# Performance work log

Measured on AMD Instinct MI355X. Metric: run time of the kernel, lower is better.

## Reference

```python
import jax, jax.numpy as jnp
import numpy as np

ALPHA = 1.0
BETA = 1.0


def setup_inputs() -> dict:
    key = jax.random.key(0)
    k1, k2, k3, k4 = jax.random.split(key, 4)
    B_, S, D_in, D_out, R = 4, 64, 8192, 8192, 16
    x = jax.random.normal(k1, (B_, S, D_in), dtype=jnp.float32)
    original_weight = jax.random.normal(k2, (D_out, D_in), dtype=jnp.float32) * 0.02
    A = jax.random.normal(k3, (D_out, R), dtype=jnp.float32) * 0.02
    Bm = jax.random.normal(k4, (R, D_in), dtype=jnp.float32) * 0.02
    return {"x": x, "original_weight": original_weight, "A": A, "B": Bm}


def reference(x, original_weight, A, B):
    # delta_weight = alpha * (A @ B)  -> [D_out, D_in]
    delta_weight = ALPHA * jnp.matmul(A, B)
    # F.linear(x, W + beta*delta) = x @ (W + beta*delta)^T
    W = original_weight + BETA * delta_weight
    return jnp.einsum("bsd,od->bso", x, W)
```

## Files before the change

### kernel.cpp

```cpp
#include <hip/hip_runtime.h>
#include <stdint.h>


#define DM 256
#define DK 8192
#define DN 8192
#define RLORA 16

#define TN 128
#define BK 64
#define KSPLIT 8
#define KCHUNK (DK / KSPLIT)
#define NITER (KCHUNK / BK)

typedef short bf16x8 __attribute__((ext_vector_type(8)));
typedef float f32x4v __attribute__((ext_vector_type(4)));

typedef __attribute__((address_space(1))) const unsigned char glbc_u8;
typedef __attribute__((address_space(3))) unsigned char lds_u8;

__device__ __forceinline__ unsigned short f2bf(float f) {
  unsigned u = __builtin_bit_cast(unsigned, f);
  u += 0x7FFFu + ((u >> 16) & 1u);
  return (unsigned short)(u >> 16);
}

__device__ __forceinline__ bf16x8 pack8(float4 a, float4 b) {
  bf16x8 r;
  r[0] = (short)f2bf(a.x); r[1] = (short)f2bf(a.y);
  r[2] = (short)f2bf(a.z); r[3] = (short)f2bf(a.w);
  r[4] = (short)f2bf(b.x); r[5] = (short)f2bf(b.y);
  r[6] = (short)f2bf(b.z); r[7] = (short)f2bf(b.w);
  return r;
}

__global__ __launch_bounds__(256) void prep_x(
    const float* __restrict__ x, const float* __restrict__ Bm,
    unsigned short* __restrict__ xb, float* __restrict__ y32) {
  const int ks = blockIdx.x;
  const int m0 = blockIdx.y * 4;
  const int t = threadIdx.x;
  const int k0 = ks * 1024 + t * 4;
  float4 xv[4];
#pragma unroll
  for (int i = 0; i < 4; ++i) {
    xv[i] = *(const float4*)(x + (size_t)(m0 + i) * DK + k0);
    ushort4 h;
    h.x = f2bf(xv[i].x); h.y = f2bf(xv[i].y);
    h.z = f2bf(xv[i].z); h.w = f2bf(xv[i].w);
    *(ushort4*)(xb + (size_t)(m0 + i) * DK + k0) = h;
  }
  float acc[4][RLORA];
#pragma unroll
  for (int r = 0; r < RLORA; ++r) {
    float4 b = *(const float4*)(Bm + (size_t)r * DK + k0);
#pragma unroll
    for (int i = 0; i < 4; ++i)
      acc[i][r] = xv[i].x * b.x + xv[i].y * b.y + xv[i].z * b.z + xv[i].w * b.w;
  }
#pragma unroll
  for (int off = 32; off >= 1; off >>= 1)
#pragma unroll
    for (int i = 0; i < 4; ++i)
#pragma unroll
      for (int r = 0; r < RLORA; ++r)
        acc[i][r] += __shfl_xor(acc[i][r], off, 64);
  __shared__ float red[4][4][RLORA];
  const int lane = t & 63, wv = t >> 6;
  if (lane == 0) {
#pragma unroll
    for (int i = 0; i < 4; ++i)
#pragma unroll
      for (int r = 0; r < RLORA; ++r) red[wv][i][r] = acc[i][r];
  }
  __syncthreads();
  if (t < 64) {
    int i = t >> 4, r = t & 15;
    float s = red[0][i][r] + red[1][i][r] + red[2][i][r] + red[3][i][r];
    atomicAdd(y32 + (m0 + i) * RLORA + r, s);
  }
}

__global__ __launch_bounds__(256) void pack_y(
    const float* __restrict__ y32, unsigned short* __restrict__ yb) {
  int e = blockIdx.x * 256 + threadIdx.x;
  int m = e >> 6, c = e & 63;
  yb[e] = (c < RLORA) ? f2bf(y32[m * RLORA + c]) : (unsigned short)0;
}

__global__ __launch_bounds__(512, 4) void lora_gemm(
    const unsigned short* __restrict__ xb,
    const float* __restrict__ W,
    const unsigned short* __restrict__ yb,
    const float* __restrict__ A,
    float* __restrict__ out,
    float* __restrict__ part) {
  __shared__ unsigned short xs[2][DM * BK];

  const int tid = threadIdx.x;
  const int lane = tid & 63;
  const int wave = tid >> 6;
  const int nb = blockIdx.x * TN;
  const int kz = blockIdx.y;
  const int kb = kz * KCHUNK;
  const int n0 = nb + wave * 16;
  const int qr = lane & 15;
  const int quad = lane >> 4;

  const unsigned short* xgp[4];
  unsigned xdst[4];
#pragma unroll
  for (int j = 0; j < 4; ++j) {
    int idx = (wave * 4 + j) * 64 + lane;
    int r = idx & 15, c = (idx >> 4) & 3, s = (idx >> 6) & 1, g = idx >> 7;
    xgp[j] = xb + (size_t)(g * 16 + r) * DK + kb + s * 32 + c * 8;
    xdst[j] = (unsigned)((wave * 4 + j) * 1024);
  }
  const float* wp = W + (size_t)(n0 + qr) * DK + kb + quad * 8;

  f32x4v acc[16];
#pragma unroll
  for (int g = 0; g < 16; ++g) acc[g] = (f32x4v){0.f, 0.f, 0.f, 0.f};

  const bool isLora = (kz == 0);
  const int niter = isLora ? NITER + 1 : NITER;

  float4 f0 = *(const float4*)(wp);
  float4 f1 = *(const float4*)(wp + 4);
  float4 f2 = *(const float4*)(wp + 32);
  float4 f3 = *(const float4*)(wp + 36);
  wp += BK;
#pragma unroll
  for (int j = 0; j < 4; ++j) {
    __builtin_amdgcn_global_load_lds((glbc_u8*)xgp[j],
        (lds_u8*)((char*)&xs[0][0] + xdst[j]), 16, 0, 0);
    xgp[j] += BK;
  }
  __syncthreads();

  for (int it = 0; it < niter; ++it) {
    const int cur = it & 1, nxt = (it + 1) & 1;
    const int ni = it + 1;
    if (ni < NITER) {
#pragma unroll
      for (int j = 0; j < 4; ++j) {
        __builtin_amdgcn_global_load_lds((glbc_u8*)xgp[j],
            (lds_u8*)((char*)&xs[nxt][0] + xdst[j]), 16, 0, 0);
        xgp[j] += BK;
      }
    } else if (ni == NITER && isLora) {
#pragma unroll
      for (int j = 0; j < 4; ++j) {
        int idx = (wave * 4 + j) * 64 + lane;
        int r = idx & 15, c = (idx >> 4) & 3, s = (idx >> 6) & 1, g = idx >> 7;
        const unsigned short* gp = yb + (g * 16 + r) * 64 + s * 32 + c * 8;
        __builtin_amdgcn_global_load_lds((glbc_u8*)gp,
            (lds_u8*)((char*)&xs[nxt][0] + xdst[j]), 16, 0, 0);
      }
    }
    bf16x8 b0 = pack8(f0, f1);
    bf16x8 b1 = pack8(f2, f3);
    if (ni < NITER) {
      f0 = *(const float4*)(wp);
      f1 = *(const float4*)(wp + 4);
      f2 = *(const float4*)(wp + 32);
      f3 = *(const float4*)(wp + 36);
      wp += BK;
    } else if (ni == NITER && isLora) {
      const float* ap = A + (size_t)(n0 + qr) * RLORA + quad * 8;
      float4 z = {0.f, 0.f, 0.f, 0.f};
      f0 = (quad < 2) ? *(const float4*)(ap) : z;
      f1 = (quad < 2) ? *(const float4*)(ap + 4) : z;
      f2 = z; f3 = z;
    }
    const char* xbase = (const char*)&xs[cur][0];
#pragma unroll
    for (int g = 0; g < 16; ++g) {
      bf16x8 a = *(const bf16x8*)(xbase + ((g * 2 + 0) * 64 + lane) * 16);
      acc[g] = __builtin_amdgcn_mfma_f32_16x16x32_bf16(a, b0, acc[g], 0, 0, 0);
    }
#pragma unroll
    for (int g = 0; g < 16; ++g) {
      bf16x8 a = *(const bf16x8*)(xbase + ((g * 2 + 1) * 64 + lane) * 16);
      acc[g] = __builtin_amdgcn_mfma_f32_16x16x32_bf16(a, b1, acc[g], 0, 0, 0);
    }
    __syncthreads();
  }

  if (part) {
    float* pb = part + (size_t)kz * DM * DN + n0 + (lane & 15);
#pragma unroll
    for (int g = 0; g < 16; ++g)
#pragma unroll
      for (int rg = 0; rg < 4; ++rg)
        pb[(size_t)(g * 16 + quad * 4 + rg) * DN] = acc[g][rg];
  } else {
    float* ob = out + n0 + (lane & 15);
#pragma unroll
    for (int g = 0; g < 16; ++g)
#pragma unroll
      for (int rg = 0; rg < 4; ++rg)
        atomicAdd(ob + (size_t)(g * 16 + quad * 4 + rg) * DN, acc[g][rg]);
  }
}

__global__ __launch_bounds__(256) void reduce_k(
    const float* __restrict__ part, float* __restrict__ out) {
  size_t i = ((size_t)blockIdx.x * 256 + threadIdx.x) * 4;
  float4 s = *(const float4*)(part + i);
#pragma unroll
  for (int kz = 1; kz < KSPLIT; ++kz) {
    float4 v = *(const float4*)(part + (size_t)kz * DM * DN + i);
    s.x += v.x; s.y += v.y; s.z += v.z; s.w += v.w;
  }
  *(float4*)(out + i) = s;
}

extern "C" void kernel_launch(void* const* d_in, const int* in_sizes, int n_in,
                              void* d_out, int out_size, void* d_ws, size_t ws_size,
                              hipStream_t stream) {
  const float* x  = (const float*)d_in[0];
  const float* W  = (const float*)d_in[1];
  const float* A  = (const float*)d_in[2];
  const float* Bm = (const float*)d_in[3];
  float* out = (float*)d_out;

  unsigned short* xb = (unsigned short*)d_ws;
  unsigned short* yb = xb + (size_t)DM * DK;
  float* y32 = (float*)(yb + (size_t)DM * 64);
  size_t base_bytes = (size_t)DM * DK * 2 + (size_t)DM * 64 * 2 +
                      (size_t)DM * RLORA * 4;
  size_t part_bytes = (size_t)KSPLIT * DM * DN * 4;
  bool use_part = ws_size >= base_bytes + part_bytes;
  float* part = use_part ? (float*)((char*)d_ws + base_bytes) : nullptr;

  hipMemsetAsync(d_out, 0, (size_t)out_size * sizeof(float), stream);
  hipMemsetAsync(y32, 0, (size_t)DM * RLORA * sizeof(float), stream);
  prep_x<<<dim3(8, 64), 256, 0, stream>>>(x, Bm, xb, y32);
  pack_y<<<64, 256, 0, stream>>>(y32, yb);
  lora_gemm<<<dim3(DN / TN, KSPLIT), 512, 0, stream>>>(xb, W, yb, A, out, part);
  if (use_part) reduce_k<<<2048, 256, 0, stream>>>(part, out);
}
```

Measured before the change: 467.0 us.

## Pre-swizzle x into MFMA fragment layout and drop LDS staging in LoRA GEMM

prep_x now writes bf16 x directly in MFMA A-fragment order, and pack_y does the same for y, so each wave can load its operands straight from global memory without LDS staging or barriers. Each wave now computes a 128x32 output tile over a K chunk, with K split into 4 parts instead of 8. That halves the partial-sum traffic in the reduce, and the output memset is skipped when partials are used. The cost is that the x fragments are re-read from global/L2 by every wave with no LDS sharing across waves, and there are more VGPRs per wave.

```diff
diff --git a/kernel.cpp b/kernel.cpp
--- a/kernel.cpp
+++ b/kernel.cpp
@@ -6,18 +6,13 @@
 #define DK 8192
 #define DN 8192
 #define RLORA 16
-
-#define TN 128
+#define KSPLIT 4
+#define KCHUNK (DK / KSPLIT)
 #define BK 64
-#define KSPLIT 8
-#define KCHUNK (DK / KSPLIT)
 #define NITER (KCHUNK / BK)
 
 typedef short bf16x8 __attribute__((ext_vector_type(8)));
 typedef float f32x4v __attribute__((ext_vector_type(4)));
-
-typedef __attribute__((address_space(1))) const unsigned char glbc_u8;
-typedef __attribute__((address_space(3))) unsigned char lds_u8;
 
 __device__ __forceinline__ unsigned short f2bf(float f) {
   unsigned u = __builtin_bit_cast(unsigned, f);
@@ -40,20 +35,25 @@
   const int ks = blockIdx.x;
   const int m0 = blockIdx.y * 4;
   const int t = threadIdx.x;
-  const int k0 = ks * 1024 + t * 4;
+  const int k = ks * 1024 + t * 4;
+  const int I = k >> 6, s = (k >> 5) & 1, oct = (k >> 3) & 3;
+  const int ebyte = (k & 4) * 2;
   float4 xv[4];
 #pragma unroll
   for (int i = 0; i < 4; ++i) {
-    xv[i] = *(const float4*)(x + (size_t)(m0 + i) * DK + k0);
+    const int m = m0 + i;
+    const int mh = m >> 7, mt = (m >> 4) & 7, r = m & 15;
+    xv[i] = *(const float4*)(x + (size_t)m * DK + k);
     ushort4 h;
     h.x = f2bf(xv[i].x); h.y = f2bf(xv[i].y);
     h.z = f2bf(xv[i].z); h.w = f2bf(xv[i].w);
-    *(ushort4*)(xb + (size_t)(m0 + i) * DK + k0) = h;
+    const int frag = ((mh * 128 + I) * 2 + s) * 8 + mt;
+    *(ushort4*)((char*)xb + (size_t)frag * 1024 + (oct * 16 + r) * 16 + ebyte) = h;
   }
   float acc[4][RLORA];
 #pragma unroll
   for (int r = 0; r < RLORA; ++r) {
-    float4 b = *(const float4*)(Bm + (size_t)r * DK + k0);
+    float4 b = *(const float4*)(Bm + (size_t)r * DK + k);
 #pragma unroll
     for (int i = 0; i < 4; ++i)
       acc[i][r] = xv[i].x * b.x + xv[i].y * b.y + xv[i].z * b.z + xv[i].w * b.w;
@@ -76,131 +76,161 @@
   __syncthreads();
   if (t < 64) {
     int i = t >> 4, r = t & 15;
-    float s = red[0][i][r] + red[1][i][r] + red[2][i][r] + red[3][i][r];
-    atomicAdd(y32 + (m0 + i) * RLORA + r, s);
+    float sum = red[0][i][r] + red[1][i][r] + red[2][i][r] + red[3][i][r];
+    atomicAdd(y32 + (m0 + i) * RLORA + r, sum);
   }
 }
 
 __global__ __launch_bounds__(256) void pack_y(
     const float* __restrict__ y32, unsigned short* __restrict__ yb) {
-  int e = blockIdx.x * 256 + threadIdx.x;
-  int m = e >> 6, c = e & 63;
-  yb[e] = (c < RLORA) ? f2bf(y32[m * RLORA + c]) : (unsigned short)0;
-}
-
-__global__ __launch_bounds__(512, 4) void lora_gemm(
+  int slot = blockIdx.x * 256 + threadIdx.x;
+  int fy = slot >> 7, q = slot & 127;
+  int lane = q >> 1, e0 = (q & 1) * 4;
+  int oct = lane >> 4, r = lane & 15;
+  int mh = fy >> 3, mt = fy & 7;
+  int m = mh * 128 + mt * 16 + r;
+  ushort4 h;
+  int c = oct * 8 + e0;
+  h.x = (c + 0 < RLORA) ? f2bf(y32[m * RLORA + c + 0]) : (unsigned short)0;
+  h.y = (c + 1 < RLORA) ? f2bf(y32[m * RLORA + c + 1]) : (unsigned short)0;
+  h.z = (c + 2 < RLORA) ? f2bf(y32[m * RLORA + c + 2]) : (unsigned short)0;
+  h.w = (c + 3 < RLORA) ? f2bf(y32[m * RLORA + c + 3]) : (unsigned short)0;
+  *(ushort4*)((char*)yb + (size_t)slot * 8) = h;
+}
+
+__global__ __launch_bounds__(256, 2) void lora_gemm(
     const unsigned short* __restrict__ xb,
     const float* __restrict__ W,
     const unsigned short* __restrict__ yb,
-    const float* __restrict__ A,
+    const float* __restrict__ Aw,
     float* __restrict__ out,
     float* __restrict__ part) {
-  __shared__ unsigned short xs[2][DM * BK];
-
   const int tid = threadIdx.x;
   const int lane = tid & 63;
   const int wave = tid >> 6;
-  const int nb = blockIdx.x * TN;
-  const int kz = blockIdx.y;
+  const int gid = blockIdx.x * 4 + wave;
+  const int nt = gid & 255;
+  const int tmp = gid >> 8;
+  const int kz = tmp & 3;
+  const int mh = tmp >> 2;
+  const int n0 = nt * 32;
   const int kb = kz * KCHUNK;
-  const int n0 = nb + wave * 16;
-  const int qr = lane & 15;
-  const int quad = lane >> 4;
-
-  const unsigned short* xgp[4];
-  unsigned xdst[4];
-#pragma unroll
-  for (int j = 0; j < 4; ++j) {
-    int idx = (wave * 4 + j) * 64 + lane;
-    int r = idx & 15, c = (idx >> 4) & 3, s = (idx >> 6) & 1, g = idx >> 7;
-    xgp[j] = xb + (size_t)(g * 16 + r) * DK + kb + s * 32 + c * 8;
-    xdst[j] = (unsigned)((wave * 4 + j) * 1024);
-  }
-  const float* wp = W + (size_t)(n0 + qr) * DK + kb + quad * 8;
-
-  f32x4v acc[16];
-#pragma unroll
-  for (int g = 0; g < 16; ++g) acc[g] = (f32x4v){0.f, 0.f, 0.f, 0.f};
-
-  const bool isLora = (kz == 0);
-  const int niter = isLora ? NITER + 1 : NITER;
-
-  float4 f0 = *(const float4*)(wp);
-  float4 f1 = *(const float4*)(wp + 4);
-  float4 f2 = *(const float4*)(wp + 32);
-  float4 f3 = *(const float4*)(wp + 36);
-  wp += BK;
-#pragma unroll
-  for (int j = 0; j < 4; ++j) {
-    __builtin_amdgcn_global_load_lds((glbc_u8*)xgp[j],
-        (lds_u8*)((char*)&xs[0][0] + xdst[j]), 16, 0, 0);
-    xgp[j] += BK;
-  }
-  __syncthreads();
-
-  for (int it = 0; it < niter; ++it) {
-    const int cur = it & 1, nxt = (it + 1) & 1;
-    const int ni = it + 1;
-    if (ni < NITER) {
-#pragma unroll
-      for (int j = 0; j < 4; ++j) {
-        __builtin_amdgcn_global_load_lds((glbc_u8*)xgp[j],
-            (lds_u8*)((char*)&xs[nxt][0] + xdst[j]), 16, 0, 0);
-        xgp[j] += BK;
-      }
-    } else if (ni == NITER && isLora) {
-#pragma unroll
-      for (int j = 0; j < 4; ++j) {
-        int idx = (wave * 4 + j) * 64 + lane;
-        int r = idx & 15, c = (idx >> 4) & 3, s = (idx >> 6) & 1, g = idx >> 7;
-        const unsigned short* gp = yb + (g * 16 + r) * 64 + s * 32 + c * 8;
-        __builtin_amdgcn_global_load_lds((glbc_u8*)gp,
-            (lds_u8*)((char*)&xs[nxt][0] + xdst[j]), 16, 0, 0);
-      }
+  const int qr = lane & 15, quad = lane >> 4;
+
+  const float* w0 = W + (size_t)(n0 + qr) * DK + kb + quad * 8;
+  const float* w1 = w0 + (size_t)16 * DK;
+  const bf16x8* ap = (const bf16x8*)xb +
+                     (size_t)(mh * 128 + kz * NITER) * 16 * 64 + lane;
+
+  f32x4v acc[8][2];
+#pragma unroll
+  for (int mt = 0; mt < 8; ++mt)
+#pragma unroll
+    for (int j = 0; j < 2; ++j) acc[mt][j] = (f32x4v){0.f, 0.f, 0.f, 0.f};
+
+  float4 F[2][2][2];
+#pragma unroll
+  for (int s = 0; s < 2; ++s)
+#pragma unroll
+    for (int h = 0; h < 2; ++h) {
+      F[0][s][h] = *(const float4*)(w0 + s * 32 + h * 4);
+      F[1][s][h] = *(const float4*)(w1 + s * 32 + h * 4);
     }
-    bf16x8 b0 = pack8(f0, f1);
-    bf16x8 b1 = pack8(f2, f3);
-    if (ni < NITER) {
-      f0 = *(const float4*)(wp);
-      f1 = *(const float4*)(wp + 4);
-      f2 = *(const float4*)(wp + 32);
-      f3 = *(const float4*)(wp + 36);
-      wp += BK;
-    } else if (ni == NITER && isLora) {
-      const float* ap = A + (size_t)(n0 + qr) * RLORA + quad * 8;
-      float4 z = {0.f, 0.f, 0.f, 0.f};
-      f0 = (quad < 2) ? *(const float4*)(ap) : z;
-      f1 = (quad < 2) ? *(const float4*)(ap + 4) : z;
-      f2 = z; f3 = z;
+
+  for (int it = 0; it < NITER - 1; ++it) {
+    bf16x8 av[16];
+#pragma unroll
+    for (int u = 0; u < 16; ++u) av[u] = ap[u * 64];
+    ap += 16 * 64;
+    bf16x8 b[2][2];
+#pragma unroll
+    for (int j = 0; j < 2; ++j)
+#pragma unroll
+      for (int s = 0; s < 2; ++s) b[j][s] = pack8(F[j][s][0], F[j][s][1]);
+    float4 g[2][2][2];
+#pragma unroll
+    for (int s = 0; s < 2; ++s)
+#pragma unroll
+      for (int h = 0; h < 2; ++h) {
+        g[0][s][h] = *(const float4*)(w0 + BK + s * 32 + h * 4);
+        g[1][s][h] = *(const float4*)(w1 + BK + s * 32 + h * 4);
+      }
+    w0 += BK; w1 += BK;
+#pragma unroll
+    for (int s = 0; s < 2; ++s)
+#pragma unroll
+      for (int mt = 0; mt < 8; ++mt) {
+        acc[mt][0] = __builtin_amdgcn_mfma_f32_16x16x32_bf16(
+            av[s * 8 + mt], b[0][s], acc[mt][0], 0, 0, 0);
+        acc[mt][1] = __builtin_amdgcn_mfma_f32_16x16x32_bf16(
+            av[s * 8 + mt], b[1][s], acc[mt][1], 0, 0, 0);
+      }
+#pragma unroll
+    for (int j = 0; j < 2; ++j)
+#pragma unroll
+      for (int s = 0; s < 2; ++s)
+#pragma unroll
+        for (int h = 0; h < 2; ++h) F[j][s][h] = g[j][s][h];
+  }
+  {
+    bf16x8 av[16];
+#pragma unroll
+    for (int u = 0; u < 16; ++u) av[u] = ap[u * 64];
+    bf16x8 b[2][2];
+#pragma unroll
+    for (int j = 0; j < 2; ++j)
+#pragma unroll
+      for (int s = 0; s < 2; ++s) b[j][s] = pack8(F[j][s][0], F[j][s][1]);
+#pragma unroll
+    for (int s = 0; s < 2; ++s)
+#pragma unroll
+      for (int mt = 0; mt < 8; ++mt) {
+        acc[mt][0] = __builtin_amdgcn_mfma_f32_16x16x32_bf16(
+            av[s * 8 + mt], b[0][s], acc[mt][0], 0, 0, 0);
+        acc[mt][1] = __builtin_amdgcn_mfma_f32_16x16x32_bf16(
+            av[s * 8 + mt], b[1][s], acc[mt][1], 0, 0, 0);
+      }
+  }
+
+  if (kz == 0) {
+    float4 z = {0.f, 0.f, 0.f, 0.f};
+    const float* a0 = Aw + (size_t)(n0 + qr) * RLORA + quad * 8;
+    const float* a1 = a0 + (size_t)16 * RLORA;
+    float4 p00 = (quad < 2) ? *(const float4*)(a0) : z;
+    float4 p01 = (quad < 2) ? *(const float4*)(a0 + 4) : z;
+    float4 p10 = (quad < 2) ? *(const float4*)(a1) : z;
+    float4 p11 = (quad < 2) ? *(const float4*)(a1 + 4) : z;
+    bf16x8 b0 = pack8(p00, p01), b1 = pack8(p10, p11);
+    const bf16x8* yp = (const bf16x8*)yb + mh * 8 * 64 + lane;
+#pragma unroll
+    for (int mt = 0; mt < 8; ++mt) {
+      bf16x8 av = yp[mt * 64];
+      acc[mt][0] = __builtin_amdgcn_mfma_f32_16x16x32_bf16(av, b0, acc[mt][0], 0, 0, 0);
+      acc[mt][1] = __builtin_amdgcn_mfma_f32_16x16x32_bf16(av, b1, acc[mt][1], 0, 0, 0);
     }
-    const char* xbase = (const char*)&xs[cur][0];
-#pragma unroll
-    for (int g = 0; g < 16; ++g) {
-      bf16x8 a = *(const bf16x8*)(xbase + ((g * 2 + 0) * 64 + lane) * 16);
-      acc[g] = __builtin_amdgcn_mfma_f32_16x16x32_bf16(a, b0, acc[g], 0, 0, 0);
-    }
-#pragma unroll
-    for (int g = 0; g < 16; ++g) {
-      bf16x8 a = *(const bf16x8*)(xbase + ((g * 2 + 1) * 64 + lane) * 16);
-      acc[g] = __builtin_amdgcn_mfma_f32_16x16x32_bf16(a, b1, acc[g], 0, 0, 0);
-    }
-    __syncthreads();
-  }
-
+  }
+
+  const size_t obase = (size_t)(mh * 128 + quad * 4) * DN + n0 + qr;
   if (part) {
-    float* pb = part + (size_t)kz * DM * DN + n0 + (lane & 15);
-#pragma unroll
-    for (int g = 0; g < 16; ++g)
-#pragma unroll
-      for (int rg = 0; rg < 4; ++rg)
-        pb[(size_t)(g * 16 + quad * 4 + rg) * DN] = acc[g][rg];
+    float* pb = part + (size_t)kz * DM * DN + obase;
+#pragma unroll
+    for (int mt = 0; mt < 8; ++mt)
+#pragma unroll
+      for (int rg = 0; rg < 4; ++rg) {
+        float* row = pb + (size_t)(mt * 16 + rg) * DN;
+        row[0] = acc[mt][0][rg];
+        row[16] = acc[mt][1][rg];
+      }
   } else {
-    float* ob = out + n0 + (lane & 15);
-#pragma unroll
-    for (int g = 0; g < 16; ++g)
-#pragma unroll
-      for (int rg = 0; rg < 4; ++rg)
-        atomicAdd(ob + (size_t)(g * 16 + quad * 4 + rg) * DN, acc[g][rg]);
+    float* ob = out + obase;
+#pragma unroll
+    for (int mt = 0; mt < 8; ++mt)
+#pragma unroll
+      for (int rg = 0; rg < 4; ++rg) {
+        float* row = ob + (size_t)(mt * 16 + rg) * DN;
+        atomicAdd(row, acc[mt][0][rg]);
+        atomicAdd(row + 16, acc[mt][1][rg]);
+      }
   }
 }
 
@@ -226,18 +256,18 @@
   float* out = (float*)d_out;
 
   unsigned short* xb = (unsigned short*)d_ws;
-  unsigned short* yb = xb + (size_t)DM * DK;
-  float* y32 = (float*)(yb + (size_t)DM * 64);
-  size_t base_bytes = (size_t)DM * DK * 2 + (size_t)DM * 64 * 2 +
-                      (size_t)DM * RLORA * 4;
+  unsigned short* yb = (unsigned short*)((char*)d_ws + (4u << 20));
+  float* y32 = (float*)((char*)yb + 16384);
+  size_t base_bytes = (4u << 20) + 16384 + 16384;
   size_t part_bytes = (size_t)KSPLIT * DM * DN * 4;
   bool use_part = ws_size >= base_bytes + part_bytes;
   float* part = use_part ? (float*)((char*)d_ws + base_bytes) : nullptr;
 
-  hipMemsetAsync(d_out, 0, (size_t)out_size * sizeof(float), stream);
+  if (!use_part)
+    hipMemsetAsync(d_out, 0, (size_t)out_size * sizeof(float), stream);
   hipMemsetAsync(y32, 0, (size_t)DM * RLORA * sizeof(float), stream);
   prep_x<<<dim3(8, 64), 256, 0, stream>>>(x, Bm, xb, y32);
-  pack_y<<<64, 256, 0, stream>>>(y32, yb);
-  lora_gemm<<<dim3(DN / TN, KSPLIT), 512, 0, stream>>>(xb, W, yb, A, out, part);
+  pack_y<<<8, 256, 0, stream>>>(y32, yb);
+  lora_gemm<<<512, 256, 0, stream>>>(xb, W, yb, A, out, part);
   if (use_part) reduce_k<<<2048, 256, 0, stream>>>(part, out);
 }
```

Measured after the change: 526.6 us. 12.8% more time.

## Retile LoRA GEMM into 2D warp tiles with LDS-staged W and pre-swizzled x

Applied to the files above, without the earlier changes.

The GEMM block now covers 256 output columns with 1024 threads arranged as a 4x4 grid of waves, each computing a 64x64 tile, so A and B fragments are reused across four MFMAs each. W is converted to bf16 and staged in double-buffered LDS instead of each wave streaming its own columns from registers. prep_x writes x directly in the MFMA fragment order so a block can copy it with contiguous global_load_lds. The output memset is dropped when the split-K partial buffer is used. The aim is to cut LDS and global traffic per MFMA, in exchange for more LDS per block, higher register pressure and fewer blocks in the grid.

```diff
diff --git a/kernel.cpp b/kernel.cpp
--- a/kernel.cpp
+++ b/kernel.cpp
@@ -7,7 +7,7 @@
 #define DN 8192
 #define RLORA 16
 
-#define TN 128
+#define TN 256
 #define BK 64
 #define KSPLIT 8
 #define KCHUNK (DK / KSPLIT)
@@ -40,20 +40,25 @@
   const int ks = blockIdx.x;
   const int m0 = blockIdx.y * 4;
   const int t = threadIdx.x;
-  const int k0 = ks * 1024 + t * 4;
+  const int k = ks * 1024 + t * 4;
+  const int it = (k >> 6) & 15, s = (k >> 5) & 1, oct = (k >> 3) & 3;
+  const int e = k & 7;
   float4 xv[4];
 #pragma unroll
   for (int i = 0; i < 4; ++i) {
-    xv[i] = *(const float4*)(x + (size_t)(m0 + i) * DK + k0);
+    const int m = m0 + i;
+    const int g = m >> 4, r = m & 15;
+    xv[i] = *(const float4*)(x + (size_t)m * DK + k);
     ushort4 h;
     h.x = f2bf(xv[i].x); h.y = f2bf(xv[i].y);
     h.z = f2bf(xv[i].z); h.w = f2bf(xv[i].w);
-    *(ushort4*)(xb + (size_t)(m0 + i) * DK + k0) = h;
+    const size_t chunk = (size_t)((ks * 16 + it) * 32 + s * 16 + g) * 64 + oct * 16 + r;
+    *(ushort4*)(xb + chunk * 8 + e) = h;
   }
   float acc[4][RLORA];
 #pragma unroll
   for (int r = 0; r < RLORA; ++r) {
-    float4 b = *(const float4*)(Bm + (size_t)r * DK + k0);
+    float4 b = *(const float4*)(Bm + (size_t)r * DK + k);
 #pragma unroll
     for (int i = 0; i < 4; ++i)
       acc[i][r] = xv[i].x * b.x + xv[i].y * b.y + xv[i].z * b.z + xv[i].w * b.w;
@@ -76,131 +81,162 @@
   __syncthreads();
   if (t < 64) {
     int i = t >> 4, r = t & 15;
-    float s = red[0][i][r] + red[1][i][r] + red[2][i][r] + red[3][i][r];
-    atomicAdd(y32 + (m0 + i) * RLORA + r, s);
+    float sum = red[0][i][r] + red[1][i][r] + red[2][i][r] + red[3][i][r];
+    atomicAdd(y32 + (m0 + i) * RLORA + r, sum);
   }
 }
 
 __global__ __launch_bounds__(256) void pack_y(
     const float* __restrict__ y32, unsigned short* __restrict__ yb) {
-  int e = blockIdx.x * 256 + threadIdx.x;
-  int m = e >> 6, c = e & 63;
-  yb[e] = (c < RLORA) ? f2bf(y32[m * RLORA + c]) : (unsigned short)0;
-}
-
-__global__ __launch_bounds__(512, 4) void lora_gemm(
+  int slot = blockIdx.x * 256 + threadIdx.x;
+  int fy = slot >> 6, l = slot & 63;
+  int oct = l >> 4, r = l & 15;
+  int m = fy * 16 + r;
+  unsigned short v[8];
+#pragma unroll
+  for (int e = 0; e < 8; ++e) {
+    int c = oct * 8 + e;
+    v[e] = (c < RLORA) ? f2bf(y32[m * RLORA + c]) : (unsigned short)0;
+  }
+  *(ushort4*)(yb + slot * 8) = make_ushort4(v[0], v[1], v[2], v[3]);
+  *(ushort4*)(yb + slot * 8 + 4) = make_ushort4(v[4], v[5], v[6], v[7]);
+}
+
+__global__ __launch_bounds__(1024) void lora_gemm(
     const unsigned short* __restrict__ xb,
     const float* __restrict__ W,
     const unsigned short* __restrict__ yb,
-    const float* __restrict__ A,
+    const float* __restrict__ Aw,
     float* __restrict__ out,
     float* __restrict__ part) {
-  __shared__ unsigned short xs[2][DM * BK];
+  __shared__ unsigned short xsm[2][16384];
+  __shared__ unsigned short wsm[2][16384];
 
   const int tid = threadIdx.x;
-  const int lane = tid & 63;
-  const int wave = tid >> 6;
-  const int nb = blockIdx.x * TN;
+  const int lane = tid & 63, w = tid >> 6;
+  const int mi = w >> 2, ni = w & 3;
+  const int qr = lane & 15, quad = lane >> 4;
+  const int n0 = blockIdx.x * TN;
   const int kz = blockIdx.y;
   const int kb = kz * KCHUNK;
-  const int n0 = nb + wave * 16;
-  const int qr = lane & 15;
-  const int quad = lane >> 4;
-
-  const unsigned short* xgp[4];
-  unsigned xdst[4];
-#pragma unroll
-  for (int j = 0; j < 4; ++j) {
-    int idx = (wave * 4 + j) * 64 + lane;
-    int r = idx & 15, c = (idx >> 4) & 3, s = (idx >> 6) & 1, g = idx >> 7;
-    xgp[j] = xb + (size_t)(g * 16 + r) * DK + kb + s * 32 + c * 8;
-    xdst[j] = (unsigned)((wave * 4 + j) * 1024);
-  }
-  const float* wp = W + (size_t)(n0 + qr) * DK + kb + quad * 8;
-
-  f32x4v acc[16];
-#pragma unroll
-  for (int g = 0; g < 16; ++g) acc[g] = (f32x4v){0.f, 0.f, 0.f, 0.f};
-
-  const bool isLora = (kz == 0);
-  const int niter = isLora ? NITER + 1 : NITER;
-
-  float4 f0 = *(const float4*)(wp);
-  float4 f1 = *(const float4*)(wp + 4);
-  float4 f2 = *(const float4*)(wp + 32);
-  float4 f3 = *(const float4*)(wp + 36);
-  wp += BK;
-#pragma unroll
-  for (int j = 0; j < 4; ++j) {
-    __builtin_amdgcn_global_load_lds((glbc_u8*)xgp[j],
-        (lds_u8*)((char*)&xs[0][0] + xdst[j]), 16, 0, 0);
-    xgp[j] += BK;
-  }
+
+  const int trow = tid >> 2;
+  const int tc = (tid & 3) * 16;
+  const float* wrow = W + (size_t)(n0 + trow) * DK + kb + tc;
+  const int ws_ = tc >> 5, q0 = (tc >> 3) & 3;
+  const unsigned wA =
+      (unsigned)(((ws_ * 16 + (trow >> 4)) * 64 + q0 * 16 + (trow & 15)) * 16);
+  const char* xg = (const char*)xb +
+      ((size_t)(kz * 16) * 32 * 64 + (size_t)(w * 2) * 64 + lane) * 16;
+  const unsigned xoff = (unsigned)(((w * 2) * 64 + lane) * 16);
+
+  f32x4v acc[4][4];
+#pragma unroll
+  for (int a = 0; a < 4; ++a)
+#pragma unroll
+    for (int b = 0; b < 4; ++b) acc[a][b] = (f32x4v){0.f, 0.f, 0.f, 0.f};
+
+  float4 g0 = *(const float4*)(wrow);
+  float4 g1 = *(const float4*)(wrow + 4);
+  float4 g2 = *(const float4*)(wrow + 8);
+  float4 g3 = *(const float4*)(wrow + 12);
+  __builtin_amdgcn_global_load_lds((glbc_u8*)xg,
+      (lds_u8*)((char*)xsm[0] + xoff), 16, 0, 0);
+  __builtin_amdgcn_global_load_lds((glbc_u8*)(xg + 1024),
+      (lds_u8*)((char*)xsm[0] + xoff + 1024), 16, 0, 0);
+  *(bf16x8*)((char*)wsm[0] + wA) = pack8(g0, g1);
+  *(bf16x8*)((char*)wsm[0] + wA + 256) = pack8(g2, g3);
   __syncthreads();
 
-  for (int it = 0; it < niter; ++it) {
-    const int cur = it & 1, nxt = (it + 1) & 1;
-    const int ni = it + 1;
-    if (ni < NITER) {
-#pragma unroll
-      for (int j = 0; j < 4; ++j) {
-        __builtin_amdgcn_global_load_lds((glbc_u8*)xgp[j],
-            (lds_u8*)((char*)&xs[nxt][0] + xdst[j]), 16, 0, 0);
-        xgp[j] += BK;
+  for (int it = 0; it < NITER; ++it) {
+    char* xcur = (char*)xsm[it & 1];
+    char* xnxt = (char*)xsm[(it + 1) & 1];
+    char* wcur = (char*)wsm[it & 1];
+    char* wnxt = (char*)wsm[(it + 1) & 1];
+    const bool havW = (it + 1 < NITER);
+    if (havW) {
+      const float* wsrc = wrow + (size_t)(it + 1) * BK;
+      g0 = *(const float4*)(wsrc);
+      g1 = *(const float4*)(wsrc + 4);
+      g2 = *(const float4*)(wsrc + 8);
+      g3 = *(const float4*)(wsrc + 12);
+      const char* xs2 = xg + (size_t)(it + 1) * 32768;
+      __builtin_amdgcn_global_load_lds((glbc_u8*)xs2,
+          (lds_u8*)(xnxt + xoff), 16, 0, 0);
+      __builtin_amdgcn_global_load_lds((glbc_u8*)(xs2 + 1024),
+          (lds_u8*)(xnxt + xoff + 1024), 16, 0, 0);
+    } else if (kz == 0) {
+      __builtin_amdgcn_global_load_lds(
+          (glbc_u8*)((const char*)yb + (w * 64 + lane) * 16),
+          (lds_u8*)(xnxt + (w * 64 + lane) * 16), 16, 0, 0);
+    }
+#pragma unroll
+    for (int s = 0; s < 2; ++s) {
+      bf16x8 a[4], b[4];
+#pragma unroll
+      for (int mt = 0; mt < 4; ++mt)
+        a[mt] = *(const bf16x8*)(xcur + (((s * 16 + mi * 4 + mt) * 64 + lane) * 16));
+#pragma unroll
+      for (int sub = 0; sub < 4; ++sub)
+        b[sub] = *(const bf16x8*)(wcur + (((s * 16 + ni * 4 + sub) * 64 + lane) * 16));
+#pragma unroll
+      for (int mt = 0; mt < 4; ++mt)
+#pragma unroll
+        for (int sub = 0; sub < 4; ++sub)
+          acc[mt][sub] = __builtin_amdgcn_mfma_f32_16x16x32_bf16(
+              a[mt], b[sub], acc[mt][sub], 0, 0, 0);
+    }
+    if (havW) {
+      *(bf16x8*)(wnxt + wA) = pack8(g0, g1);
+      *(bf16x8*)(wnxt + wA + 256) = pack8(g2, g3);
+    }
+    __syncthreads();
+  }
+
+  if (kz == 0) {
+    const char* ybase = (const char*)xsm[0];
+    bf16x8 b[4];
+    float4 z = {0.f, 0.f, 0.f, 0.f};
+#pragma unroll
+    for (int sub = 0; sub < 4; ++sub) {
+      int n_l = ni * 64 + sub * 16 + qr;
+      const float* ap = Aw + (size_t)(n0 + n_l) * RLORA + quad * 8;
+      float4 p0 = (quad < 2) ? *(const float4*)(ap) : z;
+      float4 p1 = (quad < 2) ? *(const float4*)(ap + 4) : z;
+      b[sub] = pack8(p0, p1);
+    }
+#pragma unroll
+    for (int mt = 0; mt < 4; ++mt) {
+      bf16x8 av = *(const bf16x8*)(ybase + (((mi * 4 + mt) * 64 + lane) * 16));
+#pragma unroll
+      for (int sub = 0; sub < 4; ++sub)
+        acc[mt][sub] = __builtin_amdgcn_mfma_f32_16x16x32_bf16(
+            av, b[sub], acc[mt][sub], 0, 0, 0);
+    }
+  }
+
+  if (part) {
+    float* pb = part + (size_t)kz * DM * DN;
+#pragma unroll
+    for (int mt = 0; mt < 4; ++mt)
+#pragma unroll
+      for (int sub = 0; sub < 4; ++sub) {
+        float* p = pb + (size_t)(mi * 64 + mt * 16 + quad * 4) * DN +
+                   n0 + ni * 64 + sub * 16 + qr;
+#pragma unroll
+        for (int rg = 0; rg < 4; ++rg) p[(size_t)rg * DN] = acc[mt][sub][rg];
       }
-    } else if (ni == NITER && isLora) {
-#pragma unroll
-      for (int j = 0; j < 4; ++j) {
-        int idx = (wave * 4 + j) * 64 + lane;
-        int r = idx & 15, c = (idx >> 4) & 3, s = (idx >> 6) & 1, g = idx >> 7;
-        const unsigned short* gp = yb + (g * 16 + r) * 64 + s * 32 + c * 8;
-        __builtin_amdgcn_global_load_lds((glbc_u8*)gp,
-            (lds_u8*)((char*)&xs[nxt][0] + xdst[j]), 16, 0, 0);
+  } else {
+    float* ob = out;
+#pragma unroll
+    for (int mt = 0; mt < 4; ++mt)
+#pragma unroll
+      for (int sub = 0; sub < 4; ++sub) {
+        float* p = ob + (size_t)(mi * 64 + mt * 16 + quad * 4) * DN +
+                   n0 + ni * 64 + sub * 16 + qr;
+#pragma unroll
+        for (int rg = 0; rg < 4; ++rg) atomicAdd(p + (size_t)rg * DN, acc[mt][sub][rg]);
       }
-    }
-    bf16x8 b0 = pack8(f0, f1);
-    bf16x8 b1 = pack8(f2, f3);
-    if (ni < NITER) {
-      f0 = *(const float4*)(wp);
-      f1 = *(const float4*)(wp + 4);
-      f2 = *(const float4*)(wp + 32);
-      f3 = *(const float4*)(wp + 36);
-      wp += BK;
-    } else if (ni == NITER && isLora) {
-      const float* ap = A + (size_t)(n0 + qr) * RLORA + quad * 8;
-      float4 z = {0.f, 0.f, 0.f, 0.f};
-      f0 = (quad < 2) ? *(const float4*)(ap) : z;
-      f1 = (quad < 2) ? *(const float4*)(ap + 4) : z;
-      f2 = z; f3 = z;
-    }
-    const char* xbase = (const char*)&xs[cur][0];
-#pragma unroll
-    for (int g = 0; g < 16; ++g) {
-      bf16x8 a = *(const bf16x8*)(xbase + ((g * 2 + 0) * 64 + lane) * 16);
-      acc[g] = __builtin_amdgcn_mfma_f32_16x16x32_bf16(a, b0, acc[g], 0, 0, 0);
-    }
-#pragma unroll
-    for (int g = 0; g < 16; ++g) {
-      bf16x8 a = *(const bf16x8*)(xbase + ((g * 2 + 1) * 64 + lane) * 16);
-      acc[g] = __builtin_amdgcn_mfma_f32_16x16x32_bf16(a, b1, acc[g], 0, 0, 0);
-    }
-    __syncthreads();
-  }
-
-  if (part) {
-    float* pb = part + (size_t)kz * DM * DN + n0 + (lane & 15);
-#pragma unroll
-    for (int g = 0; g < 16; ++g)
-#pragma unroll
-      for (int rg = 0; rg < 4; ++rg)
-        pb[(size_t)(g * 16 + quad * 4 + rg) * DN] = acc[g][rg];
-  } else {
-    float* ob = out + n0 + (lane & 15);
-#pragma unroll
-    for (int g = 0; g < 16; ++g)
-#pragma unroll
-      for (int rg = 0; rg < 4; ++rg)
-        atomicAdd(ob + (size_t)(g * 16 + quad * 4 + rg) * DN, acc[g][rg]);
   }
 }
 
@@ -209,8 +245,8 @@
   size_t i = ((size_t)blockIdx.x * 256 + threadIdx.x) * 4;
   float4 s = *(const float4*)(part + i);
 #pragma unroll
-  for (int kz = 1; kz < KSPLIT; ++kz) {
-    float4 v = *(const float4*)(part + (size_t)kz * DM * DN + i);
+  for (int kzi = 1; kzi < KSPLIT; ++kzi) {
+    float4 v = *(const float4*)(part + (size_t)kzi * DM * DN + i);
     s.x += v.x; s.y += v.y; s.z += v.z; s.w += v.w;
   }
   *(float4*)(out + i) = s;
@@ -226,18 +262,18 @@
   float* out = (float*)d_out;
 
   unsigned short* xb = (unsigned short*)d_ws;
-  unsigned short* yb = xb + (size_t)DM * DK;
-  float* y32 = (float*)(yb + (size_t)DM * 64);
-  size_t base_bytes = (size_t)DM * DK * 2 + (size_t)DM * 64 * 2 +
-                      (size_t)DM * RLORA * 4;
+  unsigned short* yb = (unsigned short*)((char*)d_ws + (4u << 20));
+  float* y32 = (float*)((char*)yb + 16384);
+  size_t base_bytes = (4u << 20) + 16384 + 16384;
   size_t part_bytes = (size_t)KSPLIT * DM * DN * 4;
   bool use_part = ws_size >= base_bytes + part_bytes;
   float* part = use_part ? (float*)((char*)d_ws + base_bytes) : nullptr;
 
-  hipMemsetAsync(d_out, 0, (size_t)out_size * sizeof(float), stream);
+  if (!use_part)
+    hipMemsetAsync(d_out, 0, (size_t)out_size * sizeof(float), stream);
   hipMemsetAsync(y32, 0, (size_t)DM * RLORA * sizeof(float), stream);
   prep_x<<<dim3(8, 64), 256, 0, stream>>>(x, Bm, xb, y32);
-  pack_y<<<64, 256, 0, stream>>>(y32, yb);
-  lora_gemm<<<dim3(DN / TN, KSPLIT), 512, 0, stream>>>(xb, W, yb, A, out, part);
+  pack_y<<<4, 256, 0, stream>>>(y32, yb);
+  lora_gemm<<<dim3(DN / TN, KSPLIT), 1024, 0, stream>>>(xb, W, yb, A, out, part);
   if (use_part) reduce_k<<<2048, 256, 0, stream>>>(part, out);
 }
```

Measured after the change: 452.6 us. 1.03x faster.
